# Performance work log

Measured on AMD Instinct MI355X. Metric: run time of the kernel, lower is better.

The kernel has to match this reference:

```python
import jax, jax.numpy as jnp
import numpy as np

VOCAB = 50257
EMB = 512
HID = 512


def setup_inputs() -> dict:
    key = jax.random.key(0)
    ks = jax.random.split(key, 8)
    x = jax.random.randint(ks[0], (64, 512), 0, VOCAB, dtype=jnp.int32)
    emb = jax.random.normal(ks[1], (VOCAB, EMB), dtype=jnp.float32) * 0.02
    # stacked LSTM gate weights per layer: order (i, f, o, c); Linear(in=EMB+HID or HID+HID, out=HID)
    s0 = 1.0 / np.sqrt(EMB + HID)
    s1 = 1.0 / np.sqrt(HID + HID)
    W0 = jax.random.uniform(ks[2], (4, HID, EMB + HID), jnp.float32, -s0, s0)
    b0 = jax.random.uniform(ks[3], (4, HID), jnp.float32, -s0, s0)
    W1 = jax.random.uniform(ks[4], (4, HID, HID + HID), jnp.float32, -s1, s1)
    b1 = jax.random.uniform(ks[5], (4, HID), jnp.float32, -s1, s1)
    sf = 1.0 / np.sqrt(HID)
    fc_w = jax.random.uniform(ks[6], (1, HID), jnp.float32, -sf, sf)
    fc_b = jax.random.uniform(ks[7], (1,), jnp.float32, -sf, sf)
    return {"x": x, "emb": emb, "W0": W0, "b0": b0, "W1": W1, "b1": b1,
            "fc_w": fc_w, "fc_b": fc_b}


def _lstm_cell(inp, h, c, W, b):
    # combined = [inp, h]; gates stacked (i, f, o, c); activation = relu
    combined = jnp.concatenate([inp, h], axis=-1)        # [B, In+H]
    gates = jnp.einsum('bi,ghi->bgh', combined, W) + b   # [B, 4, H]
    i_t = jax.nn.sigmoid(gates[:, 0])
    f_t = jax.nn.sigmoid(gates[:, 1])
    o_t = jax.nn.sigmoid(gates[:, 2])
    g_t = jax.nn.relu(gates[:, 3])
    c_new = f_t * c + i_t * g_t
    h_new = o_t * jax.nn.relu(c_new)
    return h_new, c_new


def reference(x, emb, W0, b0, W1, b1, fc_w, fc_b):
    B, T = x.shape
    emb_z = emb.at[0].set(0.0)          # padding_idx=0
    xe = emb_z[x]                        # [B, T, EMB]
    xe = jnp.transpose(xe, (1, 0, 2))    # [T, B, EMB]

    def step(carry, x_t):
        h0, c0, h1, c1 = carry
        h0, c0 = _lstm_cell(x_t, h0, c0, W0, b0)
        h1, c1 = _lstm_cell(h0, h1, c1, W1, b1)
        return (h0, c0, h1, c1), None

    z = jnp.zeros((B, HID), dtype=xe.dtype)
    (h0, c0, h1, c1), _ = jax.lax.scan(step, (z, z, z, z), xe)
    out = h1 @ fc_w.T + fc_b             # [B, 1]
    return jax.nn.sigmoid(out)
```

## Files before the change

kernel.cpp:

```cpp
#include <hip/hip_runtime.h>
#include <hip/hip_bf16.h>
#include <math.h>

typedef __attribute__((ext_vector_type(8))) short bf16x8;
typedef __attribute__((ext_vector_type(4))) float f32x4;

static constexpr int Tc = 512, HIDc = 512;
static constexpr int NWGc = 256, THR = 256;

static constexpr size_t WSB_H0  = 0;
static constexpr size_t WSB_H1  = WSB_H0 + 3ull * 65536;
static constexpr size_t WSB_XE  = WSB_H1 + 2ull * 65536;
static constexpr size_t WSB_CTR = WSB_XE + 3ull * 65536;
static constexpr size_t WSB_EPO = WSB_CTR + 512;
static constexpr size_t WSB_FLG = WSB_EPO + 64;
static constexpr size_t WSB_END = WSB_FLG + 256 * 64;

static constexpr unsigned FMAGIC = 0x1357acedu;
static constexpr unsigned EPBASE = 0x40000000u;
static constexpr int SPIN_CAP = 1 << 20;

__device__ __forceinline__ unsigned ld_devu(const unsigned* p) {
    return __hip_atomic_load(p, __ATOMIC_RELAXED, __HIP_MEMORY_SCOPE_AGENT);
}
__device__ __forceinline__ unsigned long long ld_devu64(const unsigned long long* p) {
    return __hip_atomic_load(p, __ATOMIC_RELAXED, __HIP_MEMORY_SCOPE_AGENT);
}
__device__ __forceinline__ void st_devu(unsigned* p, unsigned v) {
    __hip_atomic_store(p, v, __ATOMIC_RELAXED, __HIP_MEMORY_SCOPE_AGENT);
}
template<int N> __device__ __forceinline__ void s_wait_vm() {
    asm volatile("s_waitcnt vmcnt(%0)" :: "n"(N) : "memory");
}
__device__ __forceinline__ void s_wait_lgkm() {
    asm volatile("s_waitcnt lgkmcnt(0)" ::: "memory");
}
__device__ __forceinline__ void wgbar() {
    asm volatile("" ::: "memory");
    __builtin_amdgcn_s_barrier();
    asm volatile("" ::: "memory");
}
__device__ __forceinline__ unsigned short bfc(float f) {
    __hip_bfloat16 h = __float2bfloat16(f);
    return *(unsigned short*)&h;
}
__device__ __forceinline__ float bf2f(unsigned short u) {
    __hip_bfloat16 h; *(unsigned short*)&h = u;
    return __bfloat162float(h);
}

__global__ __launch_bounds__(THR, 1)
void lstm_persistent(const int* __restrict__ xp,
                     const float* __restrict__ emb,
                     const float* __restrict__ W0,
                     const float* __restrict__ b0,
                     const float* __restrict__ W1,
                     const float* __restrict__ b1,
                     const float* __restrict__ fcw,
                     const float* __restrict__ fcb,
                     float* __restrict__ out,
                     float* __restrict__ ws)
{
    char* wsc = (char*)ws;

    unsigned* ctr = (unsigned*)(wsc + WSB_CTR);
    unsigned* epo = (unsigned*)(wsc + WSB_EPO);
    unsigned* flg = (unsigned*)(wsc + WSB_FLG);

    __shared__ float preF[16 * 68];
    __shared__ float hexF[4 * 64];

    const int  tid   = threadIdx.x;
    const int  wg    = blockIdx.x;
    const bool is_l0 = (wg < 128);
    const int  hw    = (is_l0 ? wg : wg - 128) * 4;
    const float* Wb  = is_l0 ? W0 : W1;
    const float* bb  = is_l0 ? b0 : b1;
    const int  b_    = tid & 63;
    const int  wv    = __builtin_amdgcn_readfirstlane(tid >> 6);
    const int  n = tid & 15;
    const int  q = (tid & 63) >> 4;
    const size_t rowB = (size_t)(wv * 16 + n) * 1024 + (size_t)q * 16;

    if (wg == 0 && tid < 64) out[tid] = 0.25f;

    {
        unsigned long long* hz = (unsigned long long*)(wsc + WSB_H0);
        const int i = wg * THR + tid;
        if (i < 5 * 8192)
            __hip_atomic_store(hz + i, 0ull, __ATOMIC_RELAXED, __HIP_MEMORY_SCOPE_AGENT);
    }

    const int be = wg >> 1;
    const int p2 = ((wg & 1) << 7) + (tid & 127);
    auto emb_gather = [&](int wn) -> float2 {
        float2 v = make_float2(0.f, 0.f);
        if (tid < 128) {
            const int tok = xp[be * Tc + wn];
            if (tok) v = *(const float2*)(emb + (size_t)tok * 512 + p2 * 2);
        }
        return v;
    };
    auto emb_store = [&](int wn, float2 v) {
        if (tid < 128) {
            unsigned u = (unsigned)bfc(v.x) | ((unsigned)bfc(v.y) << 16);
            st_devu((unsigned*)(wsc + WSB_XE + (size_t)(wn % 3) * 65536) + be * 256 + p2, u);
        }
    };
    if (is_l0) { emb_store(0, emb_gather(0)); emb_store(1, emb_gather(1)); }

    bf16x8 bw[32];
    {
        const float* wrow = Wb + (size_t)((n >> 2) * HIDc + hw + (n & 3)) * 1024;
        #pragma unroll
        for (int f = 0; f < 32; ++f) {
            const int k0 = f * 32 + q * 8;
            const float4 u0 = *(const float4*)(wrow + k0);
            const float4 u1 = *(const float4*)(wrow + k0 + 4);
            union { unsigned short us[8]; bf16x8 v; } pk;
            pk.us[0] = bfc(u0.x); pk.us[1] = bfc(u0.y);
            pk.us[2] = bfc(u0.z); pk.us[3] = bfc(u0.w);
            pk.us[4] = bfc(u1.x); pk.us[5] = bfc(u1.y);
            pk.us[6] = bfc(u1.z); pk.us[7] = bfc(u1.w);
            bw[f] = pk.v;
        }
    }
    const float bias_n = bb[(n >> 2) * HIDc + hw + (n & 3)];

    s_wait_vm<0>();
    wgbar();
    if (tid == 0) st_devu(&flg[wg * 16], FMAGIC);
    if (wg == 0 && tid == 0) {
        for (int g = 0; g < NWGc; ++g) {
            int gu = 0;
            while (ld_devu(&flg[g * 16]) != FMAGIC && ++gu < SPIN_CAP)
                __builtin_amdgcn_s_sleep(1);
        }
        #pragma unroll
        for (int g = 0; g < 8; ++g) st_devu(&ctr[g * 16], 0u);
        s_wait_vm<0>();
        st_devu(epo, EPBASE);
    } else if (tid == 0) {
        int gu = 0;
        while (ld_devu(epo) != EPBASE && ++gu < SPIN_CAP)
            __builtin_amdgcn_s_sleep(1);
    }
    wgbar();

    float cpriv = 0.0f;

    auto ldfrag = [&](const char* slab, int cloc, int s) -> bf16x8 {
        const unsigned long long* p =
            (const unsigned long long*)(slab + rowB + (size_t)cloc * 256 + (size_t)s * 64);
        union { unsigned long long u[2]; bf16x8 v; } r;
        r.u[0] = ld_devu64(p);
        r.u[1] = ld_devu64(p + 1);
        return r.v;
    };

    #pragma unroll 1
    for (int w = 0; w <= Tc + 1; ++w) {
        const bool a0  = is_l0 && (w < Tc);
        const bool a1  = !is_l0 && (w >= 2);
        const bool act = a0 || a1;

        f32x4 acc = {0.f, 0.f, 0.f, 0.f};

        if (act) {
            const char* slabA = is_l0
                ? (wsc + WSB_XE + (size_t)(w % 3) * 65536)
                : (wsc + WSB_H0 + (size_t)((w - 2) % 3) * 65536);
            bf16x8 fa[16];
            #pragma unroll
            for (int c = 0; c < 4; ++c) {
                #pragma unroll
                for (int s = 0; s < 4; ++s)
                    fa[c * 4 + s] = ldfrag(slabA, c, s);
            }
            #pragma unroll
            for (int i = 0; i < 16; ++i)
                acc = __builtin_amdgcn_mfma_f32_16x16x32_bf16(fa[i], bw[i], acc, 0, 0, 0);
        }

        const bool ep = is_l0 && (w + 2) < Tc;
        float2 ev = make_float2(0.f, 0.f);
        if (ep) ev = emb_gather(w + 2);

        if (wg == 0) {
            if (tid == 0) {
                const unsigned tgt = (unsigned)NWGc * (unsigned)w;
                int gu = 0;
                for (;;) {
                    unsigned s = 0;
                    #pragma unroll
                    for (int g = 0; g < 8; ++g) s += ld_devu(&ctr[g * 16]);
                    if (s >= tgt || ++gu >= SPIN_CAP) break;
                }
                st_devu(epo, EPBASE + 1u + (unsigned)w);
            }
        } else {
            if (tid == 0) {
                int gu = 0;
                while (ld_devu(epo) < EPBASE + 1u + (unsigned)w && ++gu < SPIN_CAP)
                    __builtin_amdgcn_s_sleep(1);
            }
        }
        wgbar();

        if (ep) emb_store(w + 2, ev);

        if (act) {
            const char* slabB = is_l0
                ? (wsc + WSB_H0 + (size_t)((w + 2) % 3) * 65536)
                : (wsc + WSB_H1 + (size_t)((w - 3) & 1) * 65536);
            bf16x8 fb[16];
            #pragma unroll
            for (int c = 0; c < 4; ++c) {
                #pragma unroll
                for (int s = 0; s < 4; ++s)
                    fb[c * 4 + s] = ldfrag(slabB, c, s);
            }
            #pragma unroll
            for (int i = 0; i < 16; ++i)
                acc = __builtin_amdgcn_mfma_f32_16x16x32_bf16(fb[i], bw[16 + i], acc, 0, 0, 0);

            *(f32x4*)(preF + (size_t)n * 68 + wv * 16 + q * 4) = acc + bias_n;
            s_wait_lgkm(); wgbar();

            const float pI = preF[(0 * 4 + wv) * 68 + b_];
            const float pF = preF[(1 * 4 + wv) * 68 + b_];
            const float pO = preF[(2 * 4 + wv) * 68 + b_];
            const float pG = preF[(3 * 4 + wv) * 68 + b_];
            const float ig = 1.f / (1.f + expf(-pI));
            const float fg = 1.f / (1.f + expf(-pF));
            const float og = 1.f / (1.f + expf(-pO));
            const float gg = fmaxf(pG, 0.f);
            cpriv = fg * cpriv + ig * gg;
            const float hn = og * fmaxf(cpriv, 0.f);
            hexF[wv * 64 + b_] = hn;
            s_wait_lgkm(); wgbar();

            if (tid < 64) {
                unsigned long long pk = 0;
                #pragma unroll
                for (int jj = 0; jj < 4; ++jj)
                    pk |= (unsigned long long)bfc(hexF[jj * 64 + tid]) << (16 * jj);
                unsigned short* hdst = is_l0
                    ? (unsigned short*)(wsc + WSB_H0 + (size_t)(w % 3) * 65536)
                    : (unsigned short*)(wsc + WSB_H1 + (size_t)((w - 2) & 1) * 65536);
                __hip_atomic_store((unsigned long long*)(hdst + (size_t)tid * 512 + hw),
                                   pk, __ATOMIC_RELAXED, __HIP_MEMORY_SCOPE_AGENT);
            }
        }

        s_wait_vm<0>();
        wgbar();
        if (tid == 0)
            __hip_atomic_fetch_add(&ctr[(wg & 7) * 16], 1u, __ATOMIC_RELAXED,
                                   __HIP_MEMORY_SCOPE_AGENT);
    }

    if (wg == 0) {
        if (tid == 0) {
            const unsigned tgt = (unsigned)NWGc * (unsigned)(Tc + 2);
            int gu = 0;
            for (;;) {
                unsigned s = 0;
                #pragma unroll
                for (int g = 0; g < 8; ++g) s += ld_devu(&ctr[g * 16]);
                if (s >= tgt || ++gu >= SPIN_CAP) break;
            }
        }
        wgbar();
        if (tid < 64) {
            const unsigned short* h1f =
                (const unsigned short*)(wsc + WSB_H1 + (size_t)((Tc - 1) & 1) * 65536)
                + (size_t)tid * 512;
            float s = fcb[0];
            for (int h = 0; h < HIDc; h += 4) {
                const unsigned long long u = ld_devu64((const unsigned long long*)(h1f + h));
                s = fmaf(bf2f((unsigned short)(u        & 0xffff)), fcw[h + 0], s);
                s = fmaf(bf2f((unsigned short)((u >> 16) & 0xffff)), fcw[h + 1], s);
                s = fmaf(bf2f((unsigned short)((u >> 32) & 0xffff)), fcw[h + 2], s);
                s = fmaf(bf2f((unsigned short)((u >> 48) & 0xffff)), fcw[h + 3], s);
            }
            out[tid] = 1.f / (1.f + expf(-s));
        }
    }
}

extern "C" void kernel_launch(void* const* d_in, const int* in_sizes, int n_in,
                              void* d_out, int out_size, void* d_ws, size_t ws_size,
                              hipStream_t stream) {
    const int*   xp  = (const int*)d_in[0];
    const float* emb = (const float*)d_in[1];
    const float* W0  = (const float*)d_in[2];
    const float* b0  = (const float*)d_in[3];
    const float* W1  = (const float*)d_in[4];
    const float* b1  = (const float*)d_in[5];
    const float* fcw = (const float*)d_in[6];
    const float* fcb = (const float*)d_in[7];
    float* out = (float*)d_out;
    float* ws  = (float*)d_ws;

    if (ws_size < WSB_END) return;

    lstm_persistent<<<dim3(NWGc), dim3(THR), 0, stream>>>(
        xp, emb, W0, b0, W1, b1, fcw, fcb, out, ws);
}
```

Before: 5.534 ms.

## Replace per-step global barrier with per-slab readiness counters and deeper buffering

Each step's global barrier, which waited for all 256 workgroups, is replaced by per-timestep readiness counters for the h0 and h1 slabs. Each workgroup now spins only until the 128 producers of the slab it reads have published. The lagged epoch barrier now trails by two steps, and the h0, h1 and embedding ring buffers are deepened to 8, 4 and 4 slots so producers can run ahead without overwriting data still being read. The embedding gather also moves to the upper half of the threads. This adds more atomic traffic, counter polling and workspace, and makes ordering correctness depend on the buffer depths matching the allowed lag.

```diff
diff --git a/kernel.cpp b/kernel.cpp
--- a/kernel.cpp
+++ b/kernel.cpp
@@ -9,10 +9,10 @@
 static constexpr int NWGc = 256, THR = 256;
 
 static constexpr size_t WSB_H0  = 0;
-static constexpr size_t WSB_H1  = WSB_H0 + 3ull * 65536;
-static constexpr size_t WSB_XE  = WSB_H1 + 2ull * 65536;
-static constexpr size_t WSB_CTR = WSB_XE + 3ull * 65536;
-static constexpr size_t WSB_EPO = WSB_CTR + 512;
+static constexpr size_t WSB_H1  = WSB_H0 + 8ull * 65536;
+static constexpr size_t WSB_XE  = WSB_H1 + 4ull * 65536;
+static constexpr size_t WSB_CTR = WSB_XE + 4ull * 65536;
+static constexpr size_t WSB_EPO = WSB_CTR + 4608;
 static constexpr size_t WSB_FLG = WSB_EPO + 64;
 static constexpr size_t WSB_END = WSB_FLG + 256 * 64;
 
@@ -63,9 +63,11 @@
 {
     char* wsc = (char*)ws;
 
-    unsigned* ctr = (unsigned*)(wsc + WSB_CTR);
-    unsigned* epo = (unsigned*)(wsc + WSB_EPO);
-    unsigned* flg = (unsigned*)(wsc + WSB_FLG);
+    unsigned* ctrU = (unsigned*)(wsc + WSB_CTR);
+    unsigned* h0c  = ctrU + 128;
+    unsigned* h1c  = ctrU + 128 + 512;
+    unsigned* epo  = (unsigned*)(wsc + WSB_EPO);
+    unsigned* flg  = (unsigned*)(wsc + WSB_FLG);
 
     __shared__ float preF[16 * 68];
     __shared__ float hexF[4 * 64];
@@ -86,8 +88,7 @@
 
     {
         unsigned long long* hz = (unsigned long long*)(wsc + WSB_H0);
-        const int i = wg * THR + tid;
-        if (i < 5 * 8192)
+        for (int i = wg * THR + tid; i < 12 * 8192; i += NWGc * THR)
             __hip_atomic_store(hz + i, 0ull, __ATOMIC_RELAXED, __HIP_MEMORY_SCOPE_AGENT);
     }
 
@@ -95,16 +96,16 @@
     const int p2 = ((wg & 1) << 7) + (tid & 127);
     auto emb_gather = [&](int wn) -> float2 {
         float2 v = make_float2(0.f, 0.f);
-        if (tid < 128) {
+        if (tid >= 128) {
             const int tok = xp[be * Tc + wn];
             if (tok) v = *(const float2*)(emb + (size_t)tok * 512 + p2 * 2);
         }
         return v;
     };
     auto emb_store = [&](int wn, float2 v) {
-        if (tid < 128) {
+        if (tid >= 128) {
             unsigned u = (unsigned)bfc(v.x) | ((unsigned)bfc(v.y) << 16);
-            st_devu((unsigned*)(wsc + WSB_XE + (size_t)(wn % 3) * 65536) + be * 256 + p2, u);
+            st_devu((unsigned*)(wsc + WSB_XE + (size_t)(wn & 3) * 65536) + be * 256 + p2, u);
         }
     };
     if (is_l0) { emb_store(0, emb_gather(0)); emb_store(1, emb_gather(1)); }
@@ -130,20 +131,23 @@
     s_wait_vm<0>();
     wgbar();
     if (tid == 0) st_devu(&flg[wg * 16], FMAGIC);
-    if (wg == 0 && tid == 0) {
-        for (int g = 0; g < NWGc; ++g) {
-            int gu = 0;
-            while (ld_devu(&flg[g * 16]) != FMAGIC && ++gu < SPIN_CAP)
-                __builtin_amdgcn_s_sleep(1);
-        }
-        #pragma unroll
-        for (int g = 0; g < 8; ++g) st_devu(&ctr[g * 16], 0u);
+    if (wg == 0) {
+        if (tid == 0) {
+            for (int g = 0; g < NWGc; ++g) {
+                int gu = 0;
+                while (ld_devu(&flg[g * 16]) != FMAGIC && ++gu < SPIN_CAP)
+                    __builtin_amdgcn_s_sleep(1);
+            }
+        }
+        wgbar();
+        for (int i = tid; i < 1152; i += THR) st_devu(&ctrU[i], 0u);
         s_wait_vm<0>();
-        st_devu(epo, EPBASE);
-    } else if (tid == 0) {
+        wgbar();
+        if (tid == 0) st_devu(epo, EPBASE);
+    } else {
         int gu = 0;
         while (ld_devu(epo) != EPBASE && ++gu < SPIN_CAP)
-            __builtin_amdgcn_s_sleep(1);
+            __builtin_amdgcn_s_sleep(2);
     }
     wgbar();
 
@@ -157,6 +161,14 @@
         r.u[1] = ld_devu64(p + 1);
         return r.v;
     };
+    auto spin_ready = [&](const unsigned* baseU, int s) {
+        const unsigned tgt = 128u * (unsigned)((s >> 3) + 1);
+        const unsigned* p = baseU + (size_t)(s & 7) * 64;
+        int gu = 0;
+        while ((ld_devu(p) + ld_devu(p + 16) + ld_devu(p + 32) + ld_devu(p + 48)) < tgt
+               && ++gu < SPIN_CAP)
+            __builtin_amdgcn_s_sleep(1);
+    };
 
     #pragma unroll 1
     for (int w = 0; w <= Tc + 1; ++w) {
@@ -164,12 +176,36 @@
         const bool a1  = !is_l0 && (w >= 2);
         const bool act = a0 || a1;
 
+        if (w >= 2) {
+            const unsigned etgt = EPBASE + 1u + (unsigned)(w - 2);
+            if (wg == 0) {
+                if (tid == 0) {
+                    const unsigned atgt = 256u * (unsigned)(w - 1);
+                    int gu = 0;
+                    for (;;) {
+                        unsigned s = 0;
+                        #pragma unroll
+                        for (int g = 0; g < 8; ++g) s += ld_devu(&ctrU[g * 16]);
+                        if (s >= atgt || ++gu >= SPIN_CAP) break;
+                        __builtin_amdgcn_s_sleep(1);
+                    }
+                    st_devu(epo, etgt);
+                }
+                wgbar();
+            } else {
+                int gu = 0;
+                while (ld_devu(epo) < etgt && ++gu < SPIN_CAP)
+                    __builtin_amdgcn_s_sleep(2);
+            }
+        }
+
         f32x4 acc = {0.f, 0.f, 0.f, 0.f};
 
         if (act) {
+            if (a1) spin_ready(h0c, w - 2);
             const char* slabA = is_l0
-                ? (wsc + WSB_XE + (size_t)(w % 3) * 65536)
-                : (wsc + WSB_H0 + (size_t)((w - 2) % 3) * 65536);
+                ? (wsc + WSB_XE + (size_t)(w & 3) * 65536)
+                : (wsc + WSB_H0 + (size_t)((w - 2) & 7) * 65536);
             bf16x8 fa[16];
             #pragma unroll
             for (int c = 0; c < 4; ++c) {
@@ -186,33 +222,13 @@
         float2 ev = make_float2(0.f, 0.f);
         if (ep) ev = emb_gather(w + 2);
 
-        if (wg == 0) {
-            if (tid == 0) {
-                const unsigned tgt = (unsigned)NWGc * (unsigned)w;
-                int gu = 0;
-                for (;;) {
-                    unsigned s = 0;
-                    #pragma unroll
-                    for (int g = 0; g < 8; ++g) s += ld_devu(&ctr[g * 16]);
-                    if (s >= tgt || ++gu >= SPIN_CAP) break;
-                }
-                st_devu(epo, EPBASE + 1u + (unsigned)w);
-            }
-        } else {
-            if (tid == 0) {
-                int gu = 0;
-                while (ld_devu(epo) < EPBASE + 1u + (unsigned)w && ++gu < SPIN_CAP)
-                    __builtin_amdgcn_s_sleep(1);
-            }
-        }
-        wgbar();
-
-        if (ep) emb_store(w + 2, ev);
-
         if (act) {
+            if (a0) { if (w >= 1) spin_ready(h0c, w - 1); }
+            else    { if (w >= 3) spin_ready(h1c, w - 3); }
+
             const char* slabB = is_l0
-                ? (wsc + WSB_H0 + (size_t)((w + 2) % 3) * 65536)
-                : (wsc + WSB_H1 + (size_t)((w - 3) & 1) * 65536);
+                ? (wsc + WSB_H0 + (size_t)((w - 1) & 7) * 65536)
+                : (wsc + WSB_H1 + (size_t)((w - 3) & 3) * 65536);
             bf16x8 fb[16];
             #pragma unroll
             for (int c = 0; c < 4; ++c) {
@@ -246,35 +262,47 @@
                 for (int jj = 0; jj < 4; ++jj)
                     pk |= (unsigned long long)bfc(hexF[jj * 64 + tid]) << (16 * jj);
                 unsigned short* hdst = is_l0
-                    ? (unsigned short*)(wsc + WSB_H0 + (size_t)(w % 3) * 65536)
-                    : (unsigned short*)(wsc + WSB_H1 + (size_t)((w - 2) & 1) * 65536);
+                    ? (unsigned short*)(wsc + WSB_H0 + (size_t)(w & 7) * 65536)
+                    : (unsigned short*)(wsc + WSB_H1 + (size_t)((w - 2) & 3) * 65536);
                 __hip_atomic_store((unsigned long long*)(hdst + (size_t)tid * 512 + hw),
                                    pk, __ATOMIC_RELAXED, __HIP_MEMORY_SCOPE_AGENT);
-            }
-        }
+                s_wait_vm<0>();
+                if (tid == 0) {
+                    unsigned* rc = (is_l0 ? h0c : h1c)
+                        + (size_t)((is_l0 ? w : (w - 2)) & 7) * 64 + (size_t)(wg & 3) * 16;
+                    __hip_atomic_fetch_add(rc, 1u, __ATOMIC_RELAXED,
+                                           __HIP_MEMORY_SCOPE_AGENT);
+                }
+            }
+        }
+
+        if (ep) emb_store(w + 2, ev);
 
         s_wait_vm<0>();
         wgbar();
         if (tid == 0)
-            __hip_atomic_fetch_add(&ctr[(wg & 7) * 16], 1u, __ATOMIC_RELAXED,
+            __hip_atomic_fetch_add(&ctrU[(wg & 7) * 16], 1u, __ATOMIC_RELAXED,
                                    __HIP_MEMORY_SCOPE_AGENT);
     }
+
+    if (tid == 0) st_devu(&flg[wg * 16], 0u);
 
     if (wg == 0) {
         if (tid == 0) {
-            const unsigned tgt = (unsigned)NWGc * (unsigned)(Tc + 2);
+            const unsigned tgt = 256u * (unsigned)(Tc + 2);
             int gu = 0;
             for (;;) {
                 unsigned s = 0;
                 #pragma unroll
-                for (int g = 0; g < 8; ++g) s += ld_devu(&ctr[g * 16]);
+                for (int g = 0; g < 8; ++g) s += ld_devu(&ctrU[g * 16]);
                 if (s >= tgt || ++gu >= SPIN_CAP) break;
+                __builtin_amdgcn_s_sleep(1);
             }
         }
         wgbar();
         if (tid < 64) {
             const unsigned short* h1f =
-                (const unsigned short*)(wsc + WSB_H1 + (size_t)((Tc - 1) & 1) * 65536)
+                (const unsigned short*)(wsc + WSB_H1 + (size_t)((Tc - 1) & 3) * 65536)
                 + (size_t)tid * 512;
             float s = fcb[0];
             for (int h = 0; h < HIDc; h += 4) {
```

Result: slower. 5.673 ms (+2.5%).

## Gather embeddings directly per step and use inline-asm vectorized coherent slab loads

Applied to the files above, without the earlier changes.

Layer-0 workgroups now read their embedding rows straight from the fp32 table each step and convert them to bf16 in registers. This replaces the earlier staging ring, where embeddings were gathered two steps ahead into a workspace slab. Hidden-state slab loads become a single inline-asm block of sixteen dwordx4 loads with sc0 sc1 cache bits, in place of pairs of 64-bit atomic loads. The changes remove the staging stores and the pre-barrier gather, and cut the number of load instructions. In exchange, each step now issues uncoalesced fp32 embedding reads that sit on the critical path. A zero row is added for the padding token, and the completion flags are reset at kernel exit.

```diff
diff --git a/kernel.cpp b/kernel.cpp
--- a/kernel.cpp
+++ b/kernel.cpp
@@ -10,8 +10,8 @@
 
 static constexpr size_t WSB_H0  = 0;
 static constexpr size_t WSB_H1  = WSB_H0 + 3ull * 65536;
-static constexpr size_t WSB_XE  = WSB_H1 + 2ull * 65536;
-static constexpr size_t WSB_CTR = WSB_XE + 3ull * 65536;
+static constexpr size_t WSB_Z   = WSB_H1 + 2ull * 65536;
+static constexpr size_t WSB_CTR = WSB_Z + 2048;
 static constexpr size_t WSB_EPO = WSB_CTR + 512;
 static constexpr size_t WSB_FLG = WSB_EPO + 64;
 static constexpr size_t WSB_END = WSB_FLG + 256 * 64;
@@ -47,6 +47,34 @@
 __device__ __forceinline__ float bf2f(unsigned short u) {
     __hip_bfloat16 h; *(unsigned short*)&h = u;
     return __bfloat162float(h);
+}
+
+__device__ __forceinline__ void ld_slab16(const char* slab, unsigned voff,
+                                          bf16x8* f) {
+    asm volatile(
+        "global_load_dwordx4 %0, %16, %17 sc0 sc1\n\t"
+        "global_load_dwordx4 %1, %16, %17 offset:64 sc0 sc1\n\t"
+        "global_load_dwordx4 %2, %16, %17 offset:128 sc0 sc1\n\t"
+        "global_load_dwordx4 %3, %16, %17 offset:192 sc0 sc1\n\t"
+        "global_load_dwordx4 %4, %16, %17 offset:256 sc0 sc1\n\t"
+        "global_load_dwordx4 %5, %16, %17 offset:320 sc0 sc1\n\t"
+        "global_load_dwordx4 %6, %16, %17 offset:384 sc0 sc1\n\t"
+        "global_load_dwordx4 %7, %16, %17 offset:448 sc0 sc1\n\t"
+        "global_load_dwordx4 %8, %16, %17 offset:512 sc0 sc1\n\t"
+        "global_load_dwordx4 %9, %16, %17 offset:576 sc0 sc1\n\t"
+        "global_load_dwordx4 %10, %16, %17 offset:640 sc0 sc1\n\t"
+        "global_load_dwordx4 %11, %16, %17 offset:704 sc0 sc1\n\t"
+        "global_load_dwordx4 %12, %16, %17 offset:768 sc0 sc1\n\t"
+        "global_load_dwordx4 %13, %16, %17 offset:832 sc0 sc1\n\t"
+        "global_load_dwordx4 %14, %16, %17 offset:896 sc0 sc1\n\t"
+        "global_load_dwordx4 %15, %16, %17 offset:960 sc0 sc1\n\t"
+        "s_waitcnt vmcnt(0)"
+        : "=&v"(f[0]), "=&v"(f[1]), "=&v"(f[2]), "=&v"(f[3]),
+          "=&v"(f[4]), "=&v"(f[5]), "=&v"(f[6]), "=&v"(f[7]),
+          "=&v"(f[8]), "=&v"(f[9]), "=&v"(f[10]), "=&v"(f[11]),
+          "=&v"(f[12]), "=&v"(f[13]), "=&v"(f[14]), "=&v"(f[15])
+        : "v"(voff), "s"(slab)
+        : "memory");
 }
 
 __global__ __launch_bounds__(THR, 1)
@@ -66,6 +94,7 @@
     unsigned* ctr = (unsigned*)(wsc + WSB_CTR);
     unsigned* epo = (unsigned*)(wsc + WSB_EPO);
     unsigned* flg = (unsigned*)(wsc + WSB_FLG);
+    const float* zrow = (const float*)(wsc + WSB_Z);
 
     __shared__ float preF[16 * 68];
     __shared__ float hexF[4 * 64];
@@ -80,34 +109,16 @@
     const int  wv    = __builtin_amdgcn_readfirstlane(tid >> 6);
     const int  n = tid & 15;
     const int  q = (tid & 63) >> 4;
-    const size_t rowB = (size_t)(wv * 16 + n) * 1024 + (size_t)q * 16;
+    const int  b_row = wv * 16 + n;
+    const unsigned rowB = (unsigned)(b_row * 1024 + q * 16);
 
     if (wg == 0 && tid < 64) out[tid] = 0.25f;
 
     {
         unsigned long long* hz = (unsigned long long*)(wsc + WSB_H0);
-        const int i = wg * THR + tid;
-        if (i < 5 * 8192)
+        for (int i = wg * THR + tid; i < 5 * 8192 + 256; i += NWGc * THR)
             __hip_atomic_store(hz + i, 0ull, __ATOMIC_RELAXED, __HIP_MEMORY_SCOPE_AGENT);
     }
-
-    const int be = wg >> 1;
-    const int p2 = ((wg & 1) << 7) + (tid & 127);
-    auto emb_gather = [&](int wn) -> float2 {
-        float2 v = make_float2(0.f, 0.f);
-        if (tid < 128) {
-            const int tok = xp[be * Tc + wn];
-            if (tok) v = *(const float2*)(emb + (size_t)tok * 512 + p2 * 2);
-        }
-        return v;
-    };
-    auto emb_store = [&](int wn, float2 v) {
-        if (tid < 128) {
-            unsigned u = (unsigned)bfc(v.x) | ((unsigned)bfc(v.y) << 16);
-            st_devu((unsigned*)(wsc + WSB_XE + (size_t)(wn % 3) * 65536) + be * 256 + p2, u);
-        }
-    };
-    if (is_l0) { emb_store(0, emb_gather(0)); emb_store(1, emb_gather(1)); }
 
     bf16x8 bw[32];
     {
@@ -149,15 +160,6 @@
 
     float cpriv = 0.0f;
 
-    auto ldfrag = [&](const char* slab, int cloc, int s) -> bf16x8 {
-        const unsigned long long* p =
-            (const unsigned long long*)(slab + rowB + (size_t)cloc * 256 + (size_t)s * 64);
-        union { unsigned long long u[2]; bf16x8 v; } r;
-        r.u[0] = ld_devu64(p);
-        r.u[1] = ld_devu64(p + 1);
-        return r.v;
-    };
-
     #pragma unroll 1
     for (int w = 0; w <= Tc + 1; ++w) {
         const bool a0  = is_l0 && (w < Tc);
@@ -166,25 +168,32 @@
 
         f32x4 acc = {0.f, 0.f, 0.f, 0.f};
 
-        if (act) {
-            const char* slabA = is_l0
-                ? (wsc + WSB_XE + (size_t)(w % 3) * 65536)
-                : (wsc + WSB_H0 + (size_t)((w - 2) % 3) * 65536);
-            bf16x8 fa[16];
+        if (a0) {
+            const int tok = xp[b_row * Tc + w];
+            const float* er = tok ? (emb + (size_t)tok * 512) : zrow;
             #pragma unroll
             for (int c = 0; c < 4; ++c) {
                 #pragma unroll
-                for (int s = 0; s < 4; ++s)
-                    fa[c * 4 + s] = ldfrag(slabA, c, s);
-            }
+                for (int s = 0; s < 4; ++s) {
+                    const int k0 = c * 128 + s * 32 + q * 8;
+                    const float4 lo = *(const float4*)(er + k0);
+                    const float4 hi = *(const float4*)(er + k0 + 4);
+                    union { unsigned short us[8]; bf16x8 v; } pk;
+                    pk.us[0] = bfc(lo.x); pk.us[1] = bfc(lo.y);
+                    pk.us[2] = bfc(lo.z); pk.us[3] = bfc(lo.w);
+                    pk.us[4] = bfc(hi.x); pk.us[5] = bfc(hi.y);
+                    pk.us[6] = bfc(hi.z); pk.us[7] = bfc(hi.w);
+                    acc = __builtin_amdgcn_mfma_f32_16x16x32_bf16(
+                        pk.v, bw[c * 4 + s], acc, 0, 0, 0);
+                }
+            }
+        } else if (a1) {
+            bf16x8 fa[16];
+            ld_slab16(wsc + WSB_H0 + (size_t)((w - 2) % 3) * 65536, rowB, fa);
             #pragma unroll
             for (int i = 0; i < 16; ++i)
                 acc = __builtin_amdgcn_mfma_f32_16x16x32_bf16(fa[i], bw[i], acc, 0, 0, 0);
         }
-
-        const bool ep = is_l0 && (w + 2) < Tc;
-        float2 ev = make_float2(0.f, 0.f);
-        if (ep) ev = emb_gather(w + 2);
 
         if (wg == 0) {
             if (tid == 0) {
@@ -207,19 +216,12 @@
         }
         wgbar();
 
-        if (ep) emb_store(w + 2, ev);
-
         if (act) {
             const char* slabB = is_l0
                 ? (wsc + WSB_H0 + (size_t)((w + 2) % 3) * 65536)
                 : (wsc + WSB_H1 + (size_t)((w - 3) & 1) * 65536);
             bf16x8 fb[16];
-            #pragma unroll
-            for (int c = 0; c < 4; ++c) {
-                #pragma unroll
-                for (int s = 0; s < 4; ++s)
-                    fb[c * 4 + s] = ldfrag(slabB, c, s);
-            }
+            ld_slab16(slabB, rowB, fb);
             #pragma unroll
             for (int i = 0; i < 16; ++i)
                 acc = __builtin_amdgcn_mfma_f32_16x16x32_bf16(fb[i], bw[16 + i], acc, 0, 0, 0);
@@ -259,6 +261,8 @@
             __hip_atomic_fetch_add(&ctr[(wg & 7) * 16], 1u, __ATOMIC_RELAXED,
                                    __HIP_MEMORY_SCOPE_AGENT);
     }
+
+    if (tid == 0) st_devu(&flg[wg * 16], 0u);
 
     if (wg == 0) {
         if (tid == 0) {
```

New measurement: 4.982 ms. -10.0%, faster.
